# Optimization experiments

Measured on AMD Instinct MI355X. Metric: run time of the kernel, lower is better.

Reference implementation:

```python
import jax, jax.numpy as jnp
import numpy as np

N_NODES = 100000
N_EDGES = 1600000
D_IN = 64
D_OUT = 64
BN_EPS = 1e-5


def setup_inputs() -> dict:
    key = jax.random.key(0)
    k1, k2, k3 = jax.random.split(key, 3)
    x = jax.random.normal(k1, (N_NODES, D_IN), dtype=jnp.float32)
    edge_index = jax.random.randint(k2, (2, N_EDGES), 0, N_NODES, dtype=jnp.int64)
    # GCNConv linear weight [out, in], glorot-ish scale
    W = jax.random.normal(k3, (D_OUT, D_IN), dtype=jnp.float32) / np.sqrt(D_IN)
    b = jnp.zeros((D_OUT,), dtype=jnp.float32)
    gamma = jnp.ones((D_OUT,), dtype=jnp.float32)
    beta = jnp.zeros((D_OUT,), dtype=jnp.float32)
    return {"x": x, "edge_index": edge_index, "W": W, "b": b, "gamma": gamma, "beta": beta}


def reference(x, edge_index, W, b, gamma, beta):
    # --- GCNConv: h = x @ W^T, propagate with sym-normalized adjacency + self-loops ---
    h = x @ W.T  # [N, D_OUT]
    src, tgt = edge_index[0], edge_index[1]
    # degree at target nodes, +1 for self-loop
    deg = jax.ops.segment_sum(jnp.ones((src.shape[0],), h.dtype), tgt,
                              num_segments=N_NODES) + 1.0  # [N]
    dinv = jax.lax.rsqrt(deg)
    norm = dinv[src] * dinv[tgt]  # [E]
    # gather -> scale -> scatter-add; self-loop contribution is h / deg
    agg = jax.ops.segment_sum(h[src] * norm[:, None], tgt, num_segments=N_NODES)
    out = agg + h * (1.0 / deg)[:, None] + b  # [N, D_OUT]
    # --- BatchNorm1d (training-mode batch statistics, biased variance) ---
    mean = out.mean(axis=0)
    var = out.var(axis=0)
    y = gamma * (out - mean) * jax.lax.rsqrt(var + BN_EPS) + beta
    # --- ReLU (dropout = identity in eval) ---
    return jax.nn.relu(y)
```

## Files before the change

kernel.cpp:

```cpp
#include <hip/hip_runtime.h>
#include <stdint.h>

#define N_NODES_C 100000
#define N_EDGES_C 1600000
#define DIM 64
#define BN_EPS_C 1e-5f
#define BSH 7
#define NB 782
#define CH 8192

__device__ __forceinline__ int ld_idx(const void* p, int is64, size_t i) {
    if (is64) return (int)((const long long*)p)[i];
    return ((const int*)p)[i];
}

__device__ __forceinline__ int probe_is64(const unsigned int* __restrict__ p) {
    int lane = threadIdx.x & 63;
    unsigned int v = (lane < 32) ? p[2 * lane + 1] : 0u;
    return __ballot(v != 0u) == 0ull;
}

__global__ __launch_bounds__(256) void hist_kernel(const void* __restrict__ ei,
                                                   int* __restrict__ bucket_cnt) {
    __shared__ int hist[NB];
    for (int i = threadIdx.x; i < NB; i += 256) hist[i] = 0;
    __syncthreads();
    int is64 = probe_is64((const unsigned int*)ei);
    int stride = gridDim.x * blockDim.x;
    for (int e = blockIdx.x * blockDim.x + threadIdx.x; e < N_EDGES_C; e += stride) {
        int tg = ld_idx(ei, is64, (size_t)N_EDGES_C + e);
        atomicAdd(&hist[tg >> BSH], 1);
    }
    __syncthreads();
    for (int i = threadIdx.x; i < NB; i += 256) {
        int c = hist[i];
        if (c) atomicAdd(&bucket_cnt[i], c);
    }
}

__global__ __launch_bounds__(1024) void bucketscan_kernel(const int* __restrict__ bucket_cnt,
                                                          int* __restrict__ bucket_base,
                                                          int* __restrict__ bucket_cursor) {
    __shared__ int s[1024];
    int t = threadIdx.x;
    int v = (t < NB) ? bucket_cnt[t] : 0;
    s[t] = v;
    __syncthreads();
    for (int off = 1; off < 1024; off <<= 1) {
        int u = (t >= off) ? s[t - off] : 0;
        __syncthreads();
        s[t] += u;
        __syncthreads();
    }
    if (t < NB) {
        int excl = s[t] - v;
        bucket_base[t] = excl;
        bucket_cursor[t] = excl;
    }
}

__global__ __launch_bounds__(256) void binscatter_kernel(const void* __restrict__ ei,
                                                         int* __restrict__ bucket_cursor,
                                                         unsigned int* __restrict__ csr) {
    __shared__ int hist[NB];
    __shared__ int base[NB];
    int is64 = probe_is64((const unsigned int*)ei);
    int e0 = blockIdx.x * CH;
    int eend = min(e0 + CH, N_EDGES_C);
    for (int i = threadIdx.x; i < NB; i += 256) hist[i] = 0;
    __syncthreads();
    for (int e = e0 + threadIdx.x; e < eend; e += 256) {
        int tg = ld_idx(ei, is64, (size_t)N_EDGES_C + e);
        atomicAdd(&hist[tg >> BSH], 1);
    }
    __syncthreads();
    for (int i = threadIdx.x; i < NB; i += 256) {
        int c = hist[i];
        base[i] = c ? atomicAdd(&bucket_cursor[i], c) : 0;
        hist[i] = 0;
    }
    __syncthreads();
    for (int e = e0 + threadIdx.x; e < eend; e += 256) {
        int s  = ld_idx(ei, is64, (size_t)e);
        int tg = ld_idx(ei, is64, (size_t)N_EDGES_C + e);
        int b  = tg >> BSH;
        int tl = tg & 127;
        int pos = base[b] + atomicAdd(&hist[b], 1);
        csr[pos] = ((unsigned int)tl << 17) | (unsigned int)s;
    }
}

__global__ __launch_bounds__(256) void sort_kernel(const unsigned int* __restrict__ csr,
                                                   const int* __restrict__ bucket_base,
                                                   const int* __restrict__ bucket_cnt,
                                                   int* __restrict__ csr2,
                                                   int* __restrict__ rowbase,
                                                   float* __restrict__ dinv) {
    __shared__ int cnt[128];
    __shared__ int sbase[129];
    __shared__ int cur[128];
    int bk = blockIdx.x;
    int t = threadIdx.x;
    if (t < 128) cnt[t] = 0;
    __syncthreads();
    int base = bucket_base[bk], n = bucket_cnt[bk];
    for (int i = t; i < n; i += 256) {
        atomicAdd(&cnt[csr[base + i] >> 17], 1);
    }
    __syncthreads();
    if (t == 0) {
        int run = 0;
        for (int k = 0; k < 128; ++k) { sbase[k] = run; run += cnt[k]; }
        sbase[128] = run;
    }
    __syncthreads();
    if (t < 128) {
        cur[t] = base + sbase[t];
        int node = (bk << BSH) + t;
        if (node < N_NODES_C) {
            rowbase[node] = base + sbase[t];
            dinv[node] = rsqrtf((float)(cnt[t] + 1));
        }
    }
    if (bk == 0 && t == 0) rowbase[N_NODES_C] = N_EDGES_C;
    __syncthreads();
    for (int i = t; i < n; i += 256) {
        unsigned int v = csr[base + i];
        int tl = v >> 17;
        int pos = atomicAdd(&cur[tl], 1);
        csr2[pos] = (int)(v & 0x1FFFF);
    }
}

__global__ __launch_bounds__(256) void gemm_kernel(const float* __restrict__ x,
                                                   const float* __restrict__ W,
                                                   const float* __restrict__ dinv,
                                                   signed char* __restrict__ hs8,
                                                   float* __restrict__ scale) {
    __shared__ float Wl[DIM * 65];
    __shared__ float xs[32][DIM];
    int t = threadIdx.x;
    for (int i = t; i < DIM * DIM; i += 256) {
        Wl[(i >> 6) * 65 + (i & 63)] = W[i];
    }
    int r0 = blockIdx.x * 32;
    for (int i = t; i < 32 * DIM; i += 256) {
        int row = i >> 6, col = i & 63;
        int r = r0 + row;
        xs[row][col] = (r < N_NODES_C) ? x[(size_t)r * DIM + col] : 0.0f;
    }
    __syncthreads();
    int wv = t >> 6, c = t & 63;
    for (int it = 0; it < 8; ++it) {
        int rl = it * 4 + wv;
        int r = r0 + rl;
        float acc = 0.0f;
#pragma unroll
        for (int k = 0; k < DIM; ++k) acc += xs[rl][k] * Wl[c * 65 + k];
        if (r < N_NODES_C) {
            float v = acc * dinv[r];
            float m = fabsf(v);
#pragma unroll
            for (int off = 32; off >= 1; off >>= 1)
                m = fmaxf(m, __shfl_xor(m, off, 64));
            float inv = (m > 0.0f) ? 127.0f / m : 0.0f;
            int q = (int)rintf(v * inv);
            hs8[(size_t)r * DIM + c] = (signed char)q;
            if (c == 0) scale[r] = m * (1.0f / 127.0f);
        }
    }
}

__global__ __launch_bounds__(256) void gather_kernel(const int* __restrict__ csr2,
                                                     const int* __restrict__ rowbase,
                                                     const float* __restrict__ dinv,
                                                     const unsigned short* __restrict__ hsu,
                                                     const float* __restrict__ scale,
                                                     const float* __restrict__ b_,
                                                     float2* __restrict__ out,
                                                     float* __restrict__ sums,
                                                     float* __restrict__ sumsq) {
    int lane = threadIdx.x & 63;
    int half = lane >> 5;
    int c2 = lane & 31;
    int wid = blockIdx.x * (blockDim.x >> 6) + (threadIdx.x >> 6);
    int nw = gridDim.x * (blockDim.x >> 6);
    float2 bb = ((const float2*)b_)[c2];
    float s0a = 0.0f, q0a = 0.0f, s1a = 0.0f, q1a = 0.0f;

#define ISSUE8(BUF, KB)                                                        \
    _Pragma("unroll")                                                          \
    for (int k = 0; k < 8; ++k) {                                              \
        int s = __shfl(idxv, (KB) + k, 32);                                    \
        BUF[k] = (unsigned int)hsu[(size_t)s * 32 + c2];                       \
    }
#define CONSUME8(BUF, KB)                                                      \
    _Pragma("unroll")                                                          \
    for (int k = 0; k < 8; ++k) {                                              \
        bool use = ((KB) + k) < nl;                                            \
        float sc = __shfl(sclv, (KB) + k, 32);                                 \
        float scm = use ? sc : 0.0f;                                           \
        float q0 = (float)(int)(signed char)(BUF[k] & 0xFF);                   \
        float q1 = (float)(int)(signed char)(BUF[k] >> 8);                     \
        a0 = fmaf(q0, scm, a0);                                                \
        a1 = fmaf(q1, scm, a1);                                                \
    }

    for (int p = wid; p < N_NODES_C / 2; p += nw) {
        int t = 2 * p + half;
        int base = rowbase[t];
        int end = rowbase[t + 1];
        int n = end - base;
        int n_oth = __shfl_xor(n, 32, 64);
        int nmax = max(n, n_oth);
        float a0 = 0.0f, a1 = 0.0f;
        for (int kd = 0; kd < nmax; kd += 32) {
            int nl = n - kd;
            int off = (nl > 0) ? min(c2, nl - 1) : 0;
            int pos = min(base + kd + off, N_EDGES_C - 1);
            int idxv = csr2[pos];
            float sclv = scale[idxv];
            int nml = min(nmax - kd, 32);
            unsigned int uA[8], uB[8];
            ISSUE8(uA, 0);
            if (nml > 8)  { ISSUE8(uB, 8); }
            CONSUME8(uA, 0);
            if (nml > 16) { ISSUE8(uA, 16); }
            if (nml > 8)  { CONSUME8(uB, 8); }
            if (nml > 24) { ISSUE8(uB, 24); }
            if (nml > 16) { CONSUME8(uA, 16); }
            if (nml > 24) { CONSUME8(uB, 24); }
        }
        unsigned int ut = (unsigned int)hsu[(size_t)t * 32 + c2];
        float sct = scale[t];
        float qt0 = (float)(int)(signed char)(ut & 0xFF);
        float qt1 = (float)(int)(signed char)(ut >> 8);
        a0 = fmaf(qt0, sct, a0);
        a1 = fmaf(qt1, sct, a1);
        float dt = dinv[t];
        a0 = fmaf(a0, dt, bb.x);
        a1 = fmaf(a1, dt, bb.y);
        out[(size_t)t * 32 + c2] = make_float2(a0, a1);
        s0a += a0; q0a += a0 * a0;
        s1a += a1; q1a += a1 * a1;
    }
#undef ISSUE8
#undef CONSUME8

    __shared__ float r0[256], r1[256], r2[256], r3[256];
    r0[threadIdx.x] = s0a; r1[threadIdx.x] = q0a;
    r2[threadIdx.x] = s1a; r3[threadIdx.x] = q1a;
    __syncthreads();
    if (threadIdx.x < 32) {
        float S0 = 0, Q0 = 0, S1 = 0, Q1 = 0;
        for (int k = threadIdx.x; k < 256; k += 32) {
            S0 += r0[k]; Q0 += r1[k]; S1 += r2[k]; Q1 += r3[k];
        }
        unsafeAtomicAdd(&sums[2 * threadIdx.x], S0);
        unsafeAtomicAdd(&sums[2 * threadIdx.x + 1], S1);
        unsafeAtomicAdd(&sumsq[2 * threadIdx.x], Q0);
        unsafeAtomicAdd(&sumsq[2 * threadIdx.x + 1], Q1);
    }
}

__global__ __launch_bounds__(256) void bnrelu_kernel(float4* __restrict__ out,
                                                     const float* __restrict__ sums,
                                                     const float* __restrict__ sumsq,
                                                     const float* __restrict__ gamma,
                                                     const float* __restrict__ beta) {
    __shared__ float sc[DIM], sh[DIM];
    int t = threadIdx.x;
    if (t < DIM) {
        float m = sums[t] * (1.0f / N_NODES_C);
        float var = sumsq[t] * (1.0f / N_NODES_C) - m * m;
        float s = gamma[t] * rsqrtf(var + BN_EPS_C);
        sc[t] = s;
        sh[t] = beta[t] - m * s;
    }
    __syncthreads();
    const int n4 = N_NODES_C * (DIM / 4);
    int stride = gridDim.x * blockDim.x;
    for (int i = blockIdx.x * blockDim.x + t; i < n4; i += stride) {
        int cb = (i & 15) * 4;
        float4 v = out[i];
        v.x = fmaxf(fmaf(v.x, sc[cb + 0], sh[cb + 0]), 0.0f);
        v.y = fmaxf(fmaf(v.y, sc[cb + 1], sh[cb + 1]), 0.0f);
        v.z = fmaxf(fmaf(v.z, sc[cb + 2], sh[cb + 2]), 0.0f);
        v.w = fmaxf(fmaf(v.w, sc[cb + 3], sh[cb + 3]), 0.0f);
        out[i] = v;
    }
}

extern "C" void kernel_launch(void* const* d_in, const int* in_sizes, int n_in,
                              void* d_out, int out_size, void* d_ws, size_t ws_size,
                              hipStream_t stream) {
    const float* x     = (const float*)d_in[0];
    const void*  ei    = d_in[1];
    const float* W     = (const float*)d_in[2];
    const float* b     = (const float*)d_in[3];
    const float* gamma = (const float*)d_in[4];
    const float* beta  = (const float*)d_in[5];
    float* out = (float*)d_out;

    char* ws = (char*)d_ws;
    int*   bucket_cnt    = (int*)(ws + 256);
    int*   bucket_base   = (int*)(ws + 3584);
    int*   bucket_cursor = (int*)(ws + 6912);
    float* dinv          = (float*)(ws + 10240);
    int*   rowbase       = (int*)(ws + 410240);
    float* sums          = (float*)(ws + 810496);
    float* sumsq         = (float*)(ws + 810752);
    float* scale         = (float*)(ws + 811008);
    unsigned int* csr    = (unsigned int*)(ws + 1211264);
    int*   csr2          = (int*)(ws + 7611264);
    signed char* hs8     = (signed char*)(ws + 14011264);

    hipMemsetAsync(bucket_cnt, 0, NB * sizeof(int), stream);
    hipMemsetAsync(sums, 0, 512, stream);

    hist_kernel<<<256, 256, 0, stream>>>(ei, bucket_cnt);
    bucketscan_kernel<<<1, 1024, 0, stream>>>(bucket_cnt, bucket_base, bucket_cursor);
    binscatter_kernel<<<(N_EDGES_C + CH - 1) / CH, 256, 0, stream>>>(ei, bucket_cursor, csr);
    sort_kernel<<<NB, 256, 0, stream>>>(csr, bucket_base, bucket_cnt, csr2,
                                        rowbase, dinv);
    gemm_kernel<<<(N_NODES_C + 31) / 32, 256, 0, stream>>>(x, W, dinv, hs8, scale);
    gather_kernel<<<2048, 256, 0, stream>>>(csr2, rowbase, dinv,
                                            (const unsigned short*)hs8, scale, b,
                                            (float2*)out, sums, sumsq);
    bnrelu_kernel<<<1024, 256, 0, stream>>>((float4*)out, sums, sumsq, gamma, beta);
}
```

Baseline: 250.7 us.

## Split gather into two source-range passes to shrink random-access working set

The sort kernel now partitions each node's neighbor list by source index (below or above a fixed split) and stores two segment offsets per node. Gather is split into two kernels: the first aggregates neighbors from the low half of sources, and the second aggregates the high half, adds the self-loop, bias and BN statistics. The aim is to keep the randomly gathered int8 feature rows per pass small enough to stay cache-resident. The cost is an extra launch, an extra read/write of the output buffer, and twice the per-node loop overhead for short neighbor lists.

After: 274.8 us. 9.6% more time.

```diff
diff --git a/kernel.cpp b/kernel.cpp
--- a/kernel.cpp
+++ b/kernel.cpp
@@ -8,6 +8,7 @@
 #define BSH 7
 #define NB 782
 #define CH 8192
+#define TSPLIT 50000
 
 __device__ __forceinline__ int ld_idx(const void* p, int is64, size_t i) {
     if (is64) return (int)((const long long*)p)[i];
@@ -94,40 +95,44 @@
                                                    const int* __restrict__ bucket_base,
                                                    const int* __restrict__ bucket_cnt,
                                                    int* __restrict__ csr2,
-                                                   int* __restrict__ rowbase,
+                                                   int* __restrict__ seg,
                                                    float* __restrict__ dinv) {
-    __shared__ int cnt[128];
-    __shared__ int sbase[129];
-    __shared__ int cur[128];
+    __shared__ int cnt[256];
+    __shared__ int sbase[257];
+    __shared__ int cur[256];
     int bk = blockIdx.x;
     int t = threadIdx.x;
-    if (t < 128) cnt[t] = 0;
+    cnt[t] = 0;
     __syncthreads();
     int base = bucket_base[bk], n = bucket_cnt[bk];
     for (int i = t; i < n; i += 256) {
-        atomicAdd(&cnt[csr[base + i] >> 17], 1);
+        unsigned int v = csr[base + i];
+        int key = (int)(v >> 17) * 2 + ((v & 0x1FFFF) >= TSPLIT ? 1 : 0);
+        atomicAdd(&cnt[key], 1);
     }
     __syncthreads();
     if (t == 0) {
         int run = 0;
-        for (int k = 0; k < 128; ++k) { sbase[k] = run; run += cnt[k]; }
-        sbase[128] = run;
-    }
-    __syncthreads();
+        for (int k = 0; k < 256; ++k) { sbase[k] = run; run += cnt[k]; }
+        sbase[256] = run;
+    }
+    __syncthreads();
+    cur[t] = base + sbase[t];
     if (t < 128) {
-        cur[t] = base + sbase[t];
         int node = (bk << BSH) + t;
         if (node < N_NODES_C) {
-            rowbase[node] = base + sbase[t];
-            dinv[node] = rsqrtf((float)(cnt[t] + 1));
+            seg[2 * node]     = base + sbase[2 * t];
+            seg[2 * node + 1] = base + sbase[2 * t + 1];
+            int d = cnt[2 * t] + cnt[2 * t + 1];
+            dinv[node] = rsqrtf((float)(d + 1));
         }
     }
-    if (bk == 0 && t == 0) rowbase[N_NODES_C] = N_EDGES_C;
+    if (bk == 0 && t == 0) seg[2 * N_NODES_C] = N_EDGES_C;
     __syncthreads();
     for (int i = t; i < n; i += 256) {
         unsigned int v = csr[base + i];
-        int tl = v >> 17;
-        int pos = atomicAdd(&cur[tl], 1);
+        int key = (int)(v >> 17) * 2 + ((v & 0x1FFFF) >= TSPLIT ? 1 : 0);
+        int pos = atomicAdd(&cur[key], 1);
         csr2[pos] = (int)(v & 0x1FFFF);
     }
 }
@@ -171,23 +176,11 @@
     }
 }
 
-__global__ __launch_bounds__(256) void gather_kernel(const int* __restrict__ csr2,
-                                                     const int* __restrict__ rowbase,
-                                                     const float* __restrict__ dinv,
-                                                     const unsigned short* __restrict__ hsu,
-                                                     const float* __restrict__ scale,
-                                                     const float* __restrict__ b_,
-                                                     float2* __restrict__ out,
-                                                     float* __restrict__ sums,
-                                                     float* __restrict__ sumsq) {
-    int lane = threadIdx.x & 63;
-    int half = lane >> 5;
-    int c2 = lane & 31;
-    int wid = blockIdx.x * (blockDim.x >> 6) + (threadIdx.x >> 6);
-    int nw = gridDim.x * (blockDim.x >> 6);
-    float2 bb = ((const float2*)b_)[c2];
-    float s0a = 0.0f, q0a = 0.0f, s1a = 0.0f, q1a = 0.0f;
-
+__device__ __forceinline__ void gather_seg(const int* __restrict__ csr2,
+                                           const unsigned short* __restrict__ hsu,
+                                           const float* __restrict__ scale,
+                                           int base, int n, int nmax, int c2,
+                                           float& a0, float& a1) {
 #define ISSUE8(BUF, KB)                                                        \
     _Pragma("unroll")                                                          \
     for (int k = 0; k < 8; ++k) {                                              \
@@ -205,48 +198,87 @@
         a0 = fmaf(q0, scm, a0);                                                \
         a1 = fmaf(q1, scm, a1);                                                \
     }
-
+    for (int kd = 0; kd < nmax; kd += 32) {
+        int nl = n - kd;
+        int off = (nl > 0) ? min(c2, nl - 1) : 0;
+        int pos = min(base + kd + off, N_EDGES_C - 1);
+        int idxv = csr2[pos];
+        float sclv = scale[idxv];
+        int nml = min(nmax - kd, 32);
+        unsigned int uA[8], uB[8];
+        ISSUE8(uA, 0);
+        if (nml > 8)  { ISSUE8(uB, 8); }
+        CONSUME8(uA, 0);
+        if (nml > 16) { ISSUE8(uA, 16); }
+        if (nml > 8)  { CONSUME8(uB, 8); }
+        if (nml > 24) { ISSUE8(uB, 24); }
+        if (nml > 16) { CONSUME8(uA, 16); }
+        if (nml > 24) { CONSUME8(uB, 24); }
+    }
+#undef ISSUE8
+#undef CONSUME8
+}
+
+__global__ __launch_bounds__(256) void gather0_kernel(const int* __restrict__ csr2,
+                                                      const int* __restrict__ seg,
+                                                      const unsigned short* __restrict__ hsu,
+                                                      const float* __restrict__ scale,
+                                                      float2* __restrict__ out) {
+    int lane = threadIdx.x & 63;
+    int half = lane >> 5;
+    int c2 = lane & 31;
+    int wid = blockIdx.x * (blockDim.x >> 6) + (threadIdx.x >> 6);
+    int nw = gridDim.x * (blockDim.x >> 6);
     for (int p = wid; p < N_NODES_C / 2; p += nw) {
         int t = 2 * p + half;
-        int base = rowbase[t];
-        int end = rowbase[t + 1];
-        int n = end - base;
+        int base = seg[2 * t];
+        int n = seg[2 * t + 1] - base;
         int n_oth = __shfl_xor(n, 32, 64);
         int nmax = max(n, n_oth);
         float a0 = 0.0f, a1 = 0.0f;
-        for (int kd = 0; kd < nmax; kd += 32) {
-            int nl = n - kd;
-            int off = (nl > 0) ? min(c2, nl - 1) : 0;
-            int pos = min(base + kd + off, N_EDGES_C - 1);
-            int idxv = csr2[pos];
-            float sclv = scale[idxv];
-            int nml = min(nmax - kd, 32);
-            unsigned int uA[8], uB[8];
-            ISSUE8(uA, 0);
-            if (nml > 8)  { ISSUE8(uB, 8); }
-            CONSUME8(uA, 0);
-            if (nml > 16) { ISSUE8(uA, 16); }
-            if (nml > 8)  { CONSUME8(uB, 8); }
-            if (nml > 24) { ISSUE8(uB, 24); }
-            if (nml > 16) { CONSUME8(uA, 16); }
-            if (nml > 24) { CONSUME8(uB, 24); }
-        }
+        gather_seg(csr2, hsu, scale, base, n, nmax, c2, a0, a1);
+        out[(size_t)t * 32 + c2] = make_float2(a0, a1);
+    }
+}
+
+__global__ __launch_bounds__(256) void gather1_kernel(const int* __restrict__ csr2,
+                                                      const int* __restrict__ seg,
+                                                      const float* __restrict__ dinv,
+                                                      const unsigned short* __restrict__ hsu,
+                                                      const float* __restrict__ scale,
+                                                      const float* __restrict__ b_,
+                                                      float2* __restrict__ out,
+                                                      float* __restrict__ sums,
+                                                      float* __restrict__ sumsq) {
+    int lane = threadIdx.x & 63;
+    int half = lane >> 5;
+    int c2 = lane & 31;
+    int wid = blockIdx.x * (blockDim.x >> 6) + (threadIdx.x >> 6);
+    int nw = gridDim.x * (blockDim.x >> 6);
+    float2 bb = ((const float2*)b_)[c2];
+    float s0a = 0.0f, q0a = 0.0f, s1a = 0.0f, q1a = 0.0f;
+    for (int p = wid; p < N_NODES_C / 2; p += nw) {
+        int t = 2 * p + half;
+        float2 prev = out[(size_t)t * 32 + c2];
         unsigned int ut = (unsigned int)hsu[(size_t)t * 32 + c2];
         float sct = scale[t];
+        float dt = dinv[t];
+        int base = seg[2 * t + 1];
+        int n = seg[2 * t + 2] - base;
+        int n_oth = __shfl_xor(n, 32, 64);
+        int nmax = max(n, n_oth);
+        float a0 = 0.0f, a1 = 0.0f;
+        gather_seg(csr2, hsu, scale, base, n, nmax, c2, a0, a1);
         float qt0 = (float)(int)(signed char)(ut & 0xFF);
         float qt1 = (float)(int)(signed char)(ut >> 8);
-        a0 = fmaf(qt0, sct, a0);
-        a1 = fmaf(qt1, sct, a1);
-        float dt = dinv[t];
+        a0 = fmaf(qt0, sct, a0 + prev.x);
+        a1 = fmaf(qt1, sct, a1 + prev.y);
         a0 = fmaf(a0, dt, bb.x);
         a1 = fmaf(a1, dt, bb.y);
         out[(size_t)t * 32 + c2] = make_float2(a0, a1);
         s0a += a0; q0a += a0 * a0;
         s1a += a1; q1a += a1 * a1;
     }
-#undef ISSUE8
-#undef CONSUME8
-
     __shared__ float r0[256], r1[256], r2[256], r3[256];
     r0[threadIdx.x] = s0a; r1[threadIdx.x] = q0a;
     r2[threadIdx.x] = s1a; r3[threadIdx.x] = q1a;
@@ -307,13 +339,13 @@
     int*   bucket_base   = (int*)(ws + 3584);
     int*   bucket_cursor = (int*)(ws + 6912);
     float* dinv          = (float*)(ws + 10240);
-    int*   rowbase       = (int*)(ws + 410240);
-    float* sums          = (float*)(ws + 810496);
-    float* sumsq         = (float*)(ws + 810752);
-    float* scale         = (float*)(ws + 811008);
-    unsigned int* csr    = (unsigned int*)(ws + 1211264);
-    int*   csr2          = (int*)(ws + 7611264);
-    signed char* hs8     = (signed char*)(ws + 14011264);
+    int*   seg           = (int*)(ws + 410240);
+    float* sums          = (float*)(ws + 1210496);
+    float* sumsq         = (float*)(ws + 1210752);
+    float* scale         = (float*)(ws + 1211008);
+    unsigned int* csr    = (unsigned int*)(ws + 1611264);
+    int*   csr2          = (int*)(ws + 8011264);
+    signed char* hs8     = (signed char*)(ws + 14411264);
 
     hipMemsetAsync(bucket_cnt, 0, NB * sizeof(int), stream);
     hipMemsetAsync(sums, 0, 512, stream);
@@ -321,11 +353,13 @@
     hist_kernel<<<256, 256, 0, stream>>>(ei, bucket_cnt);
     bucketscan_kernel<<<1, 1024, 0, stream>>>(bucket_cnt, bucket_base, bucket_cursor);
     binscatter_kernel<<<(N_EDGES_C + CH - 1) / CH, 256, 0, stream>>>(ei, bucket_cursor, csr);
-    sort_kernel<<<NB, 256, 0, stream>>>(csr, bucket_base, bucket_cnt, csr2,
-                                        rowbase, dinv);
+    sort_kernel<<<NB, 256, 0, stream>>>(csr, bucket_base, bucket_cnt, csr2, seg, dinv);
     gemm_kernel<<<(N_NODES_C + 31) / 32, 256, 0, stream>>>(x, W, dinv, hs8, scale);
-    gather_kernel<<<2048, 256, 0, stream>>>(csr2, rowbase, dinv,
-                                            (const unsigned short*)hs8, scale, b,
-                                            (float2*)out, sums, sumsq);
+    gather0_kernel<<<2048, 256, 0, stream>>>(csr2, seg,
+                                             (const unsigned short*)hs8, scale,
+                                             (float2*)out);
+    gather1_kernel<<<2048, 256, 0, stream>>>(csr2, seg, dinv,
+                                             (const unsigned short*)hs8, scale, b,
+                                             (float2*)out, sums, sumsq);
     bnrelu_kernel<<<1024, 256, 0, stream>>>((float4*)out, sums, sumsq, gamma, beta);
 }
```
